# Kernel optimization log

Measured on AMD Instinct MI355X. Metric: run time of the kernel, lower is better.

Reference implementation:

```python
import jax, jax.numpy as jnp
import numpy as np

B, C, H, W = 4, 64, 64, 64
RC, RS = 8, 4  # channel reduction, spatial reduction
CR = C // RC
KS = 2 * RS - 1  # 7


def _conv(x, w, b, stride, pad):
    y = jax.lax.conv_general_dilated(
        x, w, (stride, stride), [(pad, pad), (pad, pad)],
        dimension_numbers=('NCHW', 'OIHW', 'NCHW'))
    return y + b[None, :, None, None]


def setup_inputs() -> dict:
    key = jax.random.key(0)
    ks = jax.random.split(key, 13)

    def w_init(k, shape):
        fan_in = shape[1] * shape[2] * shape[3]
        return jax.random.normal(k, shape, jnp.float32) / jnp.sqrt(fan_in)

    x = jax.random.normal(ks[0], (B, C, H, W), jnp.float32)
    return {
        'x': x,
        'w1': w_init(ks[1], (CR, C, 1, 1)), 'b1': jnp.zeros((CR,), jnp.float32),
        'w2': w_init(ks[2], (CR, C, 1, 1)), 'b2': jnp.zeros((CR,), jnp.float32),
        'w3': w_init(ks[3], (C, C, 1, 1)),  'b3': jnp.zeros((C,), jnp.float32),
        'w4': w_init(ks[4], (C, C, KS, KS)), 'b4': jnp.zeros((C,), jnp.float32),
        'w5': w_init(ks[5], (C, C, KS, KS)), 'b5': jnp.zeros((C,), jnp.float32),
        'w6': w_init(ks[6], (C, C, 1, 1)),  'b6': jnp.zeros((C,), jnp.float32),
    }


def reference(x, w1, b1, w2, b2, w3, b3, w4, b4, w5, b5, w6, b6):
    gamma = 1.0
    x_ori = x
    b, c, h, w = x.shape
    n = h * w

    # ---- Block 1: spatial self-attention (SAGAN-style), N x N scores ----
    f = _conv(x, w1, b1, 1, 0).reshape(b, CR, n)   # [B, C/8, N]
    g = _conv(x, w2, b2, 1, 0).reshape(b, CR, n)   # [B, C/8, N]
    hh = _conv(x, w3, b3, 1, 0).reshape(b, c, n)   # [B, C, N]
    s = jnp.einsum('bci,bcj->bij', f, g)           # [B, N, N] = f^T g
    beta = jax.nn.softmax(s, axis=1)               # softmax over dim 1 (as in torch)
    o = jnp.einsum('bcn,bnm->bcm', hh, beta)       # [B, C, N]
    x2 = o.reshape(b, c, h, w)

    # ---- Block 2: channel attention over strided-conv features, C x C scores ----
    hp, wp = h // RS, w // RS
    npix = hp * wp
    f2 = _conv(x2, w4, b4, RS, RS - 1).reshape(b, c, npix)  # [B, C, N']
    g2 = _conv(x2, w5, b5, RS, RS - 1).reshape(b, c, npix)  # [B, C, N']
    h2 = _conv(x2, w6, b6, 1, 0).reshape(b, c, n)           # [B, C, N]
    s2 = jnp.einsum('bcn,bdn->bcd', f2, g2)                 # [B, C, C] = f g^T
    beta2 = jax.nn.softmax(s2, axis=1)
    # o[b,d,n] = sum_c h2[b,c,n] * beta2[b,c,d]
    o2 = jnp.einsum('bcn,bcd->bdn', h2, beta2).reshape(b, c, h, w)

    return gamma * o2 + x_ori
```

## Files before the change

kernel.cpp:

```cpp
#include <hip/hip_runtime.h>
#include <math.h>

#define BB 4
#define CC 64
#define CRR 8
#define NN 4096

typedef __attribute__((ext_vector_type(8))) short bf16x8;
typedef __attribute__((ext_vector_type(4))) float f32x4;

__device__ inline float bf2f(ushort u) {
    union { uint i; float f; } v; v.i = (uint)u << 16; return v.f;
}
__device__ inline ushort f2bf(float f) {
    uint u = __builtin_bit_cast(uint, f);
    u = (u + 0x7FFFu + ((u >> 16) & 1u)) >> 16;
    return (ushort)u;
}
__device__ inline uint bfpack2(float a, float b) {
    uint ua = __builtin_bit_cast(uint, a);
    uint ub = __builtin_bit_cast(uint, b);
    ua = (ua + 0x7FFFu + ((ua >> 16) & 1u)) >> 16;
    ub = (ub + 0x7FFFu + ((ub >> 16) & 1u)) & 0xFFFF0000u;
    return ua | ub;
}
__device__ inline uint pkrtz(float a, float b) {
    return __builtin_amdgcn_perm(__builtin_bit_cast(uint, b),
                                 __builtin_bit_cast(uint, a), 0x07060302u);
}
__device__ inline float fexp2(float x) { return exp2f(x); }

#define X2P_B 313600

__global__ __launch_bounds__(256) void produce_fgh(
    const float* __restrict__ x,
    const float* __restrict__ w1, const float* __restrict__ b1,
    const float* __restrict__ w2, const float* __restrict__ b2,
    const float* __restrict__ w3, const float* __restrict__ b3,
    ushort* __restrict__ fT, ushort* __restrict__ gT, ushort* __restrict__ hhb)
{
    const float LOG2E = 1.4426950408889634f;
    int t = threadIdx.x;
    int b = blockIdx.x & 3;
    int n = ((blockIdx.x >> 2) << 6) + (t & 63);
    int og = __builtin_amdgcn_readfirstlane(t >> 6);

    const float* xb = x + ((size_t)b << 18) + n;
    float xv[64];
#pragma unroll
    for (int c = 0; c < 64; ++c) xv[c] = xb[(size_t)c << 12];

    if (og == 0) {
        ushort fo[8], go[8];
#pragma unroll
        for (int k = 0; k < 8; ++k) {
            float a1 = b1[k], a2 = b2[k];
#pragma unroll
            for (int c = 0; c < 64; ++c) {
                a1 = fmaf(w1[k * 64 + c], xv[c], a1);
                a2 = fmaf(w2[k * 64 + c], xv[c], a2);
            }
            fo[k] = f2bf(a1 * LOG2E); go[k] = f2bf(a2);
        }
        uint4 fq = make_uint4((uint)fo[0] | ((uint)fo[1] << 16),
                              (uint)fo[2] | ((uint)fo[3] << 16),
                              (uint)fo[4] | ((uint)fo[5] << 16),
                              (uint)fo[6] | ((uint)fo[7] << 16));
        uint4 gq = make_uint4((uint)go[0] | ((uint)go[1] << 16),
                              (uint)go[2] | ((uint)go[3] << 16),
                              (uint)go[4] | ((uint)go[5] << 16),
                              (uint)go[6] | ((uint)go[7] << 16));
        *(uint4*)&fT[((size_t)b << 15) + (size_t)n * 8] = fq;
        *(uint4*)&gT[((size_t)b << 15) + (size_t)n * 8] = gq;
#pragma unroll
        for (int k = 0; k < 4; ++k) {
            float a = b3[k];
#pragma unroll
            for (int c = 0; c < 64; ++c) a = fmaf(w3[k * 64 + c], xv[c], a);
            hhb[((size_t)b << 18) + ((size_t)k << 12) + n] = f2bf(a);
        }
    } else {
        int c0 = og * 20 - 16;
#pragma unroll
        for (int k = 0; k < 20; ++k) {
            float a = b3[c0 + k];
#pragma unroll
            for (int c = 0; c < 64; ++c) a = fmaf(w3[(c0 + k) * 64 + c], xv[c], a);
            hhb[((size_t)b << 18) + ((size_t)(c0 + k) << 12) + n] = f2bf(a);
        }
    }
}

__global__ __launch_bounds__(256) void wtz_kernel(
    const float* __restrict__ w4, const float* __restrict__ w5,
    const float* __restrict__ w6,
    ushort* __restrict__ Wt, ushort* __restrict__ w6b, ushort* __restrict__ x2p)
{
    int bid = blockIdx.x;
    int t = threadIdx.x;
    if (bid < 128) {
        int conv = bid >> 6, co = bid & 63;
        const float* W = conv ? w5 : w4;
        for (int i = t; i < 3136; i += 256) {
            int ci = i / 49, kk = i - ci * 49;
            Wt[(((size_t)(conv * 64 + co)) * 49 + kk) * 64 + ci] = f2bf(W[co * 3136 + i]);
        }
    } else if (bid == 128) {
#pragma unroll
        for (int k = 0; k < 16; ++k) {
            int i = k * 256 + t;
            w6b[i] = f2bf(w6[i]);
        }
    } else {
        int gid = (bid - 129) * 256 + t;
        if (gid >= 4 * 804) return;
        int b = gid / 804;
        int i = gid - b * 804;
        int py, px;
        if (i < 210) { py = i / 70; px = i - py * 70; }
        else if (i < 420) { int j = i - 210; int r = j / 70; py = 67 + r; px = j - r * 70; }
        else { int j = i - 420; int r = j / 6; py = 3 + r; int c = j - r * 6; px = c < 3 ? c : 64 + c; }
        ushort* p = x2p + (size_t)b * X2P_B + (size_t)(py * 70 + px) * 64;
        uint4 z = make_uint4(0, 0, 0, 0);
#pragma unroll
        for (int k = 0; k < 8; ++k) *(uint4*)(p + k * 8) = z;
    }
}

__global__ __launch_bounds__(1024) void attn_kernel(
    const ushort* __restrict__ fT, const ushort* __restrict__ gT,
    const ushort* __restrict__ hhb, const ushort* __restrict__ w6b,
    const float* __restrict__ b6,
    ushort* __restrict__ x2p, ushort* __restrict__ h2b)
{
    __shared__ __align__(16) char smem[98304];
    ushort* hhT = (ushort*)smem;
    ushort* PstB = (ushort*)(smem + 65536);
    float* Acc = (float*)smem;
    float* Lq  = (float*)(smem + 69632);
    ushort* x2s = (ushort*)(smem + 70656);

    int t = threadIdx.x;
    int q = t >> 8, tq = t & 255;
    int l = t & 63;
    int wq = tq >> 6;
    int w16 = t >> 6;
    int ml = l & 15, g = l >> 4;
    int b = blockIdx.x & 3;
    int mt = blockIdx.x >> 2;
    int m0 = mt << 6;
    int col = m0 + wq * 16 + ml;

    const ushort* fTb = fT + ((size_t)b << 15) + (size_t)q * 8192;
    const ushort* gTb = gT + ((size_t)b << 15);
    const ushort* hhB = hhb + ((size_t)b << 18) + (q << 10);

    const bf16x8 z8 = {0, 0, 0, 0, 0, 0, 0, 0};
    const f32x4 z4 = {0.f, 0.f, 0.f, 0.f};

    bf16x8 gfrag = *(const bf16x8*)(gTb + (size_t)col * 8);
    if (g != 0) gfrag = z8;

    int sc = tq >> 2, sp = tq & 3;
    const ushort* hrowBase = hhB + (size_t)sc * 4096 + sp * 16;
    int hdst = q * 8192 + sp * 1024 + sc * 8;

    uint4 h0 = *(const uint4*)(hrowBase);
    uint4 h1 = *(const uint4*)(hrowBase + 8);
    *(uint4*)&hhT[hdst] = h0;
    *(uint4*)&hhT[hdst + 512] = h1;
    bf16x8 afc[4];
#pragma unroll
    for (int s = 0; s < 4; ++s)
        afc[s] = *(const bf16x8*)(fTb + (size_t)(16 * s + ml) * 8);

    f32x4 acc[4] = {z4, z4, z4, z4};
    float rsum = 0.f;
    int swz = (ml & 7) << 4;
    char* pbase = (char*)PstB + w16 * 2048;
    __syncthreads();

    for (int nt = 0; nt < 16; ++nt) {
        int buf = nt & 1;
        bf16x8 afn[4];
        if (nt < 15) {
            int n0 = (nt + 1) << 6;
            h0 = *(const uint4*)(hrowBase + n0);
            h1 = *(const uint4*)(hrowBase + n0 + 8);
#pragma unroll
            for (int s = 0; s < 4; ++s)
                afn[s] = *(const bf16x8*)(fTb + (size_t)(n0 + 16 * s + ml) * 8);
        }

        f32x4 Sv[4];
#pragma unroll
        for (int s = 0; s < 4; ++s)
            Sv[s] = __builtin_amdgcn_mfma_f32_16x16x32_bf16(afc[s], gfrag, z4, 0, 0, 0);

        uint plo[4], phi[4];
#pragma unroll
        for (int s = 0; s < 4; ++s) {
            float p0 = fexp2(Sv[s][0]);
            float p1 = fexp2(Sv[s][1]);
            float p2 = fexp2(Sv[s][2]);
            float p3 = fexp2(Sv[s][3]);
            rsum += (p0 + p1) + (p2 + p3);
            plo[s] = pkrtz(p0, p1);
            phi[s] = pkrtz(p2, p3);
        }

#pragma unroll
        for (int s = 0; s < 4; ++s) {
            uint off = (uint)((ml * 128 + 32 * s + 8 * g) ^ swz);
            *(uint2*)(pbase + off) = make_uint2(plo[s], phi[s]);
        }

#pragma unroll
        for (int kk = 0; kk < 2; ++kk) {
            uint off = (uint)((ml * 128 + 64 * kk + 16 * g) ^ swz);
            bf16x8 pf = *(const bf16x8*)(pbase + off);
#pragma unroll
            for (int ct = 0; ct < 4; ++ct) {
                bf16x8 hf = *(const bf16x8*)&hhT[q * 8192 + buf * 4096 + (kk * 4 + g) * 512 + (16 * ct + ml) * 8];
                acc[ct] = __builtin_amdgcn_mfma_f32_16x16x32_bf16(hf, pf, acc[ct], 0, 0, 0);
            }
        }

        if (nt < 15) {
            int nb = (nt + 1) & 1;
            *(uint4*)&hhT[hdst + nb * 4096] = h0;
            *(uint4*)&hhT[hdst + nb * 4096 + 512] = h1;
#pragma unroll
            for (int s = 0; s < 4; ++s) afc[s] = afn[s];
        }
        __syncthreads();
    }

    rsum += __shfl_xor(rsum, 16);
    rsum += __shfl_xor(rsum, 32);

    {
        float* arow = Acc + q * 4352 + (wq * 16 + ml) * 68;
#pragma unroll
        for (int ct = 0; ct < 4; ++ct)
            *(f32x4*)(arow + 16 * ct + 4 * g) = acc[ct];
        if (g == 0) Lq[q * 64 + wq * 16 + ml] = rsum;
    }
    __syncthreads();

    {
        int m = t >> 4, c0 = (t & 15) << 2;
        float Ltot = Lq[m] + Lq[64 + m] + Lq[128 + m] + Lq[192 + m];
        float rL = 1.f / Ltot;
        f32x4 v0 = *(const f32x4*)(Acc + 0 * 4352 + m * 68 + c0);
        f32x4 v1 = *(const f32x4*)(Acc + 1 * 4352 + m * 68 + c0);
        f32x4 v2 = *(const f32x4*)(Acc + 2 * 4352 + m * 68 + c0);
        f32x4 v3 = *(const f32x4*)(Acc + 3 * 4352 + m * 68 + c0);
        f32x4 v;
#pragma unroll
        for (int r = 0; r < 4; ++r)
            v[r] = ((v0[r] + v1[r]) + (v2[r] + v3[r])) * rL;
        uint2 pk = make_uint2(bfpack2(v[0], v[1]), bfpack2(v[2], v[3]));
        int px = m + 3, py = mt + 3;
        *(uint2*)(x2p + (size_t)b * X2P_B + (size_t)(py * 70 + px) * 64 + c0) = pk;
        *(uint2*)(x2s + m * 72 + c0) = pk;
    }
    __syncthreads();

    {
        int dt = w16 & 3, mq = w16 >> 2;
        f32x4 hacc = z4;
#pragma unroll
        for (int kk = 0; kk < 2; ++kk) {
            bf16x8 xf = *(const bf16x8*)(x2s + (mq * 16 + ml) * 72 + 32 * kk + 8 * g);
            bf16x8 wf = *(const bf16x8*)(w6b + (size_t)(16 * dt + ml) * 64 + 32 * kk + 8 * g);
            hacc = __builtin_amdgcn_mfma_f32_16x16x32_bf16(wf, xf, hacc, 0, 0, 0);
        }
        ushort* h2row = h2b + ((size_t)b << 18) + (m0 + mq * 16 + ml);
#pragma unroll
        for (int r = 0; r < 4; ++r) {
            int d = 16 * dt + 4 * g + r;
            h2row[(size_t)d << 12] = f2bf(hacc[r] + b6[d]);
        }
    }
}

__global__ __launch_bounds__(256) void conv7_split_kernel(
    const ushort* __restrict__ x2p, const ushort* __restrict__ Wt,
    float* __restrict__ part)
{
    int t = threadIdx.x;
    int l = t & 63, w = t >> 6;
    int ml = l & 15, g = l >> 4;
    int lb = (blockIdx.x & 7) * 28 + (blockIdx.x >> 3);
    int bc = lb / 28;
    int idx = (lb % 28) * 4 + w;
    int ky = idx >> 4;
    int ct = (idx >> 2) & 3;
    int og = idx & 3;
    int conv = bc & 1, b = bc >> 1;

    int co0 = ct * 16;
    const ushort* wb = Wt + (size_t)conv * 200704
                     + (size_t)(co0 + ml) * 3136 + (size_t)(ky * 7) * 64 + g * 8;
    const ushort* xbase = x2p + (size_t)b * X2P_B + g * 8;

    int pixoff[4];
#pragma unroll
    for (int s = 0; s < 4; ++s) {
        int opix = og * 64 + s * 16 + ml;
        int oy = opix >> 4, ox = opix & 15;
        pixoff[s] = ((oy * 4 + ky) * 70 + ox * 4) * 64;
    }

    const f32x4 z4 = {0.f, 0.f, 0.f, 0.f};
    f32x4 acc[4] = {z4, z4, z4, z4};

#pragma unroll
    for (int kx = 0; kx < 7; ++kx) {
#pragma unroll
        for (int ci0 = 0; ci0 < 64; ci0 += 32) {
            bf16x8 av = *(const bf16x8*)(wb + kx * 64 + ci0);
#pragma unroll
            for (int s = 0; s < 4; ++s) {
                bf16x8 bv = *(const bf16x8*)(xbase + pixoff[s] + kx * 64 + ci0);
                acc[s] = __builtin_amdgcn_mfma_f32_16x16x32_bf16(av, bv, acc[s], 0, 0, 0);
            }
        }
    }

    float* pb = part + (size_t)(ky * 8 + bc) * 16384;
#pragma unroll
    for (int s = 0; s < 4; ++s) {
        int opix = og * 64 + s * 16 + ml;
#pragma unroll
        for (int r = 0; r < 4; ++r) {
            int co = co0 + 4 * g + r;
            pb[co * 256 + opix] = acc[s][r];
        }
    }
}

__global__ __launch_bounds__(256) void conv7_reduce_kernel(
    const float* __restrict__ part, const float* __restrict__ b4,
    const float* __restrict__ b5, float* __restrict__ f2, float* __restrict__ g2)
{
    int idx = (blockIdx.x * 256 + threadIdx.x) * 4;
    int bc = idx >> 14;
    int co = (idx >> 8) & 63;
    int conv = bc & 1, b = bc >> 1;
    int sub = idx & 16383;
    float4 s = make_float4(0.f, 0.f, 0.f, 0.f);
#pragma unroll
    for (int ky = 0; ky < 7; ++ky) {
        float4 v = *(const float4*)&part[(size_t)(ky * 8 + bc) * 16384 + sub];
        s.x += v.x; s.y += v.y; s.z += v.z; s.w += v.w;
    }
    float bias = (conv ? b5 : b4)[co];
    s.x += bias; s.y += bias; s.z += bias; s.w += bias;
    float* y = conv ? g2 : f2;
    *(float4*)&y[(size_t)b * 16384 + sub] = s;
}

__global__ __launch_bounds__(1024) void s2_softmax_kernel(
    const float* __restrict__ f2, const float* __restrict__ g2,
    float* __restrict__ beta2)
{
    __shared__ __align__(16) float g2t[4][64][68];
    __shared__ __align__(16) float s2f[64][68];
    __shared__ float red[6][64];
    int t = threadIdx.x;
    int b = blockIdx.x;
    int q = t >> 8, tq = t & 255;
    int nb = q * 64;

    {
        int n = tq & 63, c0 = tq >> 6;
#pragma unroll
        for (int k = 0; k < 16; ++k) {
            int cc = c0 * 16 + k;
            g2t[q][n][cc] = g2[((size_t)(b * 64 + cc) << 8) + nb + n];
        }
    }
    __syncthreads();

    int c = tq & 63, dq = tq >> 6, d0 = dq * 16;
    float acc[16];
#pragma unroll
    for (int k = 0; k < 16; ++k) acc[k] = 0.f;
    const float* frow = f2 + ((size_t)(b * 64 + c) << 8) + nb;
#pragma unroll 4
    for (int n = 0; n < 64; ++n) {
        float fv = frow[n];
#pragma unroll
        for (int jj = 0; jj < 4; ++jj) {
            float4 gv = *(const float4*)&g2t[q][n][d0 + jj * 4];
            acc[jj * 4 + 0] = fmaf(fv, gv.x, acc[jj * 4 + 0]);
            acc[jj * 4 + 1] = fmaf(fv, gv.y, acc[jj * 4 + 1]);
            acc[jj * 4 + 2] = fmaf(fv, gv.z, acc[jj * 4 + 2]);
            acc[jj * 4 + 3] = fmaf(fv, gv.w, acc[jj * 4 + 3]);
        }
    }
    __syncthreads();
    float* part = &g2t[0][0][0];
#pragma unroll
    for (int k = 0; k < 16; ++k) part[q * 4096 + c * 64 + d0 + k] = acc[k];
    __syncthreads();
    {
        int idx = t * 4;
        int cc = idx >> 6, dd = idx & 63;
        float4 s0 = *(const float4*)&part[cc * 64 + dd];
        float4 s1 = *(const float4*)&part[4096 + cc * 64 + dd];
        float4 s2v = *(const float4*)&part[8192 + cc * 64 + dd];
        float4 s3 = *(const float4*)&part[12288 + cc * 64 + dd];
        float4 s;
        s.x = (s0.x + s1.x) + (s2v.x + s3.x);
        s.y = (s0.y + s1.y) + (s2v.y + s3.y);
        s.z = (s0.z + s1.z) + (s2v.z + s3.z);
        s.w = (s0.w + s1.w) + (s2v.w + s3.w);
        *(float4*)&s2f[cc][dd] = s;
    }
    __syncthreads();
    if (t < 256) {
        int d = t & 63, cq = t >> 6;
        float mx = -3e38f;
#pragma unroll
        for (int k = 0; k < 16; ++k) mx = fmaxf(mx, s2f[cq * 16 + k][d]);
        red[cq][d] = mx;
    }
    __syncthreads();
    if (t < 64)
        red[4][t] = fmaxf(fmaxf(red[0][t], red[1][t]), fmaxf(red[2][t], red[3][t]));
    __syncthreads();
    if (t < 256) {
        int d = t & 63, cq = t >> 6;
        float mx = red[4][d];
        float s = 0.f;
#pragma unroll
        for (int k = 0; k < 16; ++k) s += __expf(s2f[cq * 16 + k][d] - mx);
        red[cq][d] = s;
    }
    __syncthreads();
    if (t < 64)
        red[5][t] = 1.f / ((red[0][t] + red[1][t]) + (red[2][t] + red[3][t]));
    __syncthreads();
    if (t < 256) {
        int d = t & 63, cq = t >> 6;
        float mx = red[4][d], r = red[5][d];
#pragma unroll
        for (int k = 0; k < 16; ++k) {
            int cc = cq * 16 + k;
            beta2[((size_t)b << 12) + cc * 64 + d] = __expf(s2f[cc][d] - mx) * r;
        }
    }
}

__global__ __launch_bounds__(256) void o2_residual_kernel(
    const ushort* __restrict__ h2b, const float* __restrict__ beta2,
    const float* __restrict__ x, float* __restrict__ out)
{
    __shared__ __align__(16) float b2s[64][64];
    __shared__ float h2s[64][65];
    int t = threadIdx.x;
    int b = blockIdx.x & 3;
    int n0 = (blockIdx.x >> 2) << 6;

    {
#pragma unroll
        for (int k = 0; k < 16; ++k) {
            int idx = k * 256 + t;
            b2s[idx >> 6][idx & 63] = beta2[((size_t)b << 12) + idx];
        }
        int n = t & 63; int c0 = t >> 6;
#pragma unroll
        for (int k = 0; k < 16; ++k) {
            int cc = c0 * 16 + k;
            h2s[cc][n] = bf2f(h2b[((size_t)(b * 64 + cc) << 12) + n0 + n]);
        }
    }
    __syncthreads();

    int n = t & 63, dg = t >> 6, d0 = dg * 16;
    float acc[16];
#pragma unroll
    for (int k = 0; k < 16; ++k) acc[k] = 0.f;

    for (int cc = 0; cc < 64; ++cc) {
        float hv = h2s[cc][n];
#pragma unroll
        for (int jj = 0; jj < 4; ++jj) {
            float4 bv = *reinterpret_cast<const float4*>(&b2s[cc][d0 + jj * 4]);
            acc[jj * 4 + 0] = fmaf(hv, bv.x, acc[jj * 4 + 0]);
            acc[jj * 4 + 1] = fmaf(hv, bv.y, acc[jj * 4 + 1]);
            acc[jj * 4 + 2] = fmaf(hv, bv.z, acc[jj * 4 + 2]);
            acc[jj * 4 + 3] = fmaf(hv, bv.w, acc[jj * 4 + 3]);
        }
    }
#pragma unroll
    for (int k = 0; k < 16; ++k) {
        int d = d0 + k;
        size_t o = ((size_t)(b * 64 + d) << 12) + n0 + n;
        out[o] = acc[k] + x[o];
    }
}

extern "C" void kernel_launch(void* const* d_in, const int* in_sizes, int n_in,
                              void* d_out, int out_size, void* d_ws, size_t ws_size,
                              hipStream_t stream)
{
    const float* x  = (const float*)d_in[0];
    const float* w1 = (const float*)d_in[1];
    const float* b1 = (const float*)d_in[2];
    const float* w2 = (const float*)d_in[3];
    const float* b2 = (const float*)d_in[4];
    const float* w3 = (const float*)d_in[5];
    const float* b3 = (const float*)d_in[6];
    const float* w4 = (const float*)d_in[7];
    const float* b4 = (const float*)d_in[8];
    const float* w5 = (const float*)d_in[9];
    const float* b5 = (const float*)d_in[10];
    const float* w6 = (const float*)d_in[11];
    const float* b6 = (const float*)d_in[12];
    float* out = (float*)d_out;

    ushort* u = (ushort*)d_ws;
    ushort* fT  = u;
    ushort* gT  = fT + 131072;
    ushort* hhb = gT + 131072;
    ushort* x2p = hhb + 1048576;
    ushort* h2b = x2p + 1254400;
    ushort* Wt  = h2b + 1048576;
    ushort* w6b = Wt + 401408;
    float* fr    = (float*)(w6b + 4096);
    float* f2    = fr;
    float* g2    = fr + 65536;
    float* beta2 = fr + 131072;
    float* part  = fr + 147456;

    produce_fgh<<<256, 256, 0, stream>>>(x, w1, b1, w2, b2, w3, b3, fT, gT, hhb);
    wtz_kernel<<<142, 256, 0, stream>>>(w4, w5, w6, Wt, w6b, x2p);
    attn_kernel<<<256, 1024, 0, stream>>>(fT, gT, hhb, w6b, b6, x2p, h2b);
    conv7_split_kernel<<<224, 256, 0, stream>>>(x2p, Wt, part);
    conv7_reduce_kernel<<<128, 256, 0, stream>>>(part, b4, b5, f2, g2);
    s2_softmax_kernel<<<BB, 1024, 0, stream>>>(f2, g2, beta2);
    o2_residual_kernel<<<256, 256, 0, stream>>>(h2b, beta2, x, out);
}
```

Baseline: 86.22 us.

## Split attention into partial-sum and combine kernels; merge weight prep into producer

The 1024-thread attention kernel, which reduced four key-range quarters through shared memory, is replaced by 1024 blocks of 256 threads. Each block writes fp32 partial accumulators and row sums to global memory, and a separate combine kernel sums them, normalizes, writes x2, and runs the w6 1x1 conv. The weight transpose and padding-zero kernel is folded into the producer launch as extra blocks, removing one launch. This trades smaller blocks with more occupancy and less shared memory for about 16MB of extra global partial traffic and one more kernel launch.

```diff
diff --git a/kernel.cpp b/kernel.cpp
--- a/kernel.cpp
+++ b/kernel.cpp
@@ -32,17 +32,53 @@
 
 #define X2P_B 313600
 
-__global__ __launch_bounds__(256) void produce_fgh(
+__global__ __launch_bounds__(256) void produce_wtz_kernel(
     const float* __restrict__ x,
     const float* __restrict__ w1, const float* __restrict__ b1,
     const float* __restrict__ w2, const float* __restrict__ b2,
     const float* __restrict__ w3, const float* __restrict__ b3,
-    ushort* __restrict__ fT, ushort* __restrict__ gT, ushort* __restrict__ hhb)
+    const float* __restrict__ w4, const float* __restrict__ w5,
+    const float* __restrict__ w6,
+    ushort* __restrict__ fT, ushort* __restrict__ gT, ushort* __restrict__ hhb,
+    ushort* __restrict__ Wt, ushort* __restrict__ w6b, ushort* __restrict__ x2p)
 {
     const float LOG2E = 1.4426950408889634f;
     int t = threadIdx.x;
-    int b = blockIdx.x & 3;
-    int n = ((blockIdx.x >> 2) << 6) + (t & 63);
+    int bid0 = blockIdx.x;
+    if (bid0 >= 256) {
+        int bid = bid0 - 256;
+        if (bid < 128) {
+            int conv = bid >> 6, co = bid & 63;
+            const float* W = conv ? w5 : w4;
+            for (int i = t; i < 3136; i += 256) {
+                int ci = i / 49, kk = i - ci * 49;
+                Wt[(((size_t)(conv * 64 + co)) * 49 + kk) * 64 + ci] = f2bf(W[co * 3136 + i]);
+            }
+        } else if (bid == 128) {
+#pragma unroll
+            for (int k = 0; k < 16; ++k) {
+                int i = k * 256 + t;
+                w6b[i] = f2bf(w6[i]);
+            }
+        } else {
+            int gid = (bid - 129) * 256 + t;
+            if (gid >= 4 * 804) return;
+            int b = gid / 804;
+            int i = gid - b * 804;
+            int py, px;
+            if (i < 210) { py = i / 70; px = i - py * 70; }
+            else if (i < 420) { int j = i - 210; int r = j / 70; py = 67 + r; px = j - r * 70; }
+            else { int j = i - 420; int r = j / 6; py = 3 + r; int c = j - r * 6; px = c < 3 ? c : 64 + c; }
+            ushort* p = x2p + (size_t)b * X2P_B + (size_t)(py * 70 + px) * 64;
+            uint4 z = make_uint4(0, 0, 0, 0);
+#pragma unroll
+            for (int k = 0; k < 8; ++k) *(uint4*)(p + k * 8) = z;
+        }
+        return;
+    }
+
+    int b = bid0 & 3;
+    int n = ((bid0 >> 2) << 6) + (t & 63);
     int og = __builtin_amdgcn_readfirstlane(t >> 6);
 
     const float* xb = x + ((size_t)b << 18) + n;
@@ -91,65 +127,23 @@
     }
 }
 
-__global__ __launch_bounds__(256) void wtz_kernel(
-    const float* __restrict__ w4, const float* __restrict__ w5,
-    const float* __restrict__ w6,
-    ushort* __restrict__ Wt, ushort* __restrict__ w6b, ushort* __restrict__ x2p)
-{
+__global__ __launch_bounds__(256) void attn_part_kernel(
+    const ushort* __restrict__ fT, const ushort* __restrict__ gT,
+    const ushort* __restrict__ hhb,
+    float* __restrict__ pacc, float* __restrict__ pL)
+{
+    __shared__ __align__(16) ushort hhT[8192];
+    __shared__ __align__(16) ushort Pst[4096];
+
+    int t = threadIdx.x;
+    int l = t & 63, w = t >> 6;
+    int ml = l & 15, g = l >> 4;
     int bid = blockIdx.x;
-    int t = threadIdx.x;
-    if (bid < 128) {
-        int conv = bid >> 6, co = bid & 63;
-        const float* W = conv ? w5 : w4;
-        for (int i = t; i < 3136; i += 256) {
-            int ci = i / 49, kk = i - ci * 49;
-            Wt[(((size_t)(conv * 64 + co)) * 49 + kk) * 64 + ci] = f2bf(W[co * 3136 + i]);
-        }
-    } else if (bid == 128) {
-#pragma unroll
-        for (int k = 0; k < 16; ++k) {
-            int i = k * 256 + t;
-            w6b[i] = f2bf(w6[i]);
-        }
-    } else {
-        int gid = (bid - 129) * 256 + t;
-        if (gid >= 4 * 804) return;
-        int b = gid / 804;
-        int i = gid - b * 804;
-        int py, px;
-        if (i < 210) { py = i / 70; px = i - py * 70; }
-        else if (i < 420) { int j = i - 210; int r = j / 70; py = 67 + r; px = j - r * 70; }
-        else { int j = i - 420; int r = j / 6; py = 3 + r; int c = j - r * 6; px = c < 3 ? c : 64 + c; }
-        ushort* p = x2p + (size_t)b * X2P_B + (size_t)(py * 70 + px) * 64;
-        uint4 z = make_uint4(0, 0, 0, 0);
-#pragma unroll
-        for (int k = 0; k < 8; ++k) *(uint4*)(p + k * 8) = z;
-    }
-}
-
-__global__ __launch_bounds__(1024) void attn_kernel(
-    const ushort* __restrict__ fT, const ushort* __restrict__ gT,
-    const ushort* __restrict__ hhb, const ushort* __restrict__ w6b,
-    const float* __restrict__ b6,
-    ushort* __restrict__ x2p, ushort* __restrict__ h2b)
-{
-    __shared__ __align__(16) char smem[98304];
-    ushort* hhT = (ushort*)smem;
-    ushort* PstB = (ushort*)(smem + 65536);
-    float* Acc = (float*)smem;
-    float* Lq  = (float*)(smem + 69632);
-    ushort* x2s = (ushort*)(smem + 70656);
-
-    int t = threadIdx.x;
-    int q = t >> 8, tq = t & 255;
-    int l = t & 63;
-    int wq = tq >> 6;
-    int w16 = t >> 6;
-    int ml = l & 15, g = l >> 4;
-    int b = blockIdx.x & 3;
-    int mt = blockIdx.x >> 2;
+    int b = bid & 3;
+    int mt = (bid >> 2) & 63;
+    int q = bid >> 8;
     int m0 = mt << 6;
-    int col = m0 + wq * 16 + ml;
+    int col = m0 + w * 16 + ml;
 
     const ushort* fTb = fT + ((size_t)b << 15) + (size_t)q * 8192;
     const ushort* gTb = gT + ((size_t)b << 15);
@@ -161,9 +155,9 @@
     bf16x8 gfrag = *(const bf16x8*)(gTb + (size_t)col * 8);
     if (g != 0) gfrag = z8;
 
-    int sc = tq >> 2, sp = tq & 3;
+    int sc = t >> 2, sp = t & 3;
     const ushort* hrowBase = hhB + (size_t)sc * 4096 + sp * 16;
-    int hdst = q * 8192 + sp * 1024 + sc * 8;
+    int hdst = sp * 1024 + sc * 8;
 
     uint4 h0 = *(const uint4*)(hrowBase);
     uint4 h1 = *(const uint4*)(hrowBase + 8);
@@ -177,7 +171,7 @@
     f32x4 acc[4] = {z4, z4, z4, z4};
     float rsum = 0.f;
     int swz = (ml & 7) << 4;
-    char* pbase = (char*)PstB + w16 * 2048;
+    char* pbase = (char*)&Pst[0] + w * 2048;
     __syncthreads();
 
     for (int nt = 0; nt < 16; ++nt) {
@@ -221,7 +215,7 @@
             bf16x8 pf = *(const bf16x8*)(pbase + off);
 #pragma unroll
             for (int ct = 0; ct < 4; ++ct) {
-                bf16x8 hf = *(const bf16x8*)&hhT[q * 8192 + buf * 4096 + (kk * 4 + g) * 512 + (16 * ct + ml) * 8];
+                bf16x8 hf = *(const bf16x8*)&hhT[buf * 4096 + (kk * 4 + g) * 512 + (16 * ct + ml) * 8];
                 acc[ct] = __builtin_amdgcn_mfma_f32_16x16x32_bf16(hf, pf, acc[ct], 0, 0, 0);
             }
         }
@@ -240,47 +234,71 @@
     rsum += __shfl_xor(rsum, 32);
 
     {
-        float* arow = Acc + q * 4352 + (wq * 16 + ml) * 68;
+        int m = w * 16 + ml;
+        float* pb = pacc + (size_t)bid * 4096 + m * 64;
 #pragma unroll
         for (int ct = 0; ct < 4; ++ct)
-            *(f32x4*)(arow + 16 * ct + 4 * g) = acc[ct];
-        if (g == 0) Lq[q * 64 + wq * 16 + ml] = rsum;
-    }
-    __syncthreads();
+            *(f32x4*)(pb + 16 * ct + 4 * g) = acc[ct];
+        if (g == 0) pL[(size_t)bid * 64 + m] = rsum;
+    }
+}
+
+__global__ __launch_bounds__(256) void attn_combine_kernel(
+    const float* __restrict__ pacc, const float* __restrict__ pL,
+    const ushort* __restrict__ w6b, const float* __restrict__ b6,
+    ushort* __restrict__ x2p, ushort* __restrict__ h2b)
+{
+    __shared__ __align__(16) ushort x2s[64 * 72];
+    int t = threadIdx.x;
+    int cid = blockIdx.x;
+    int b = cid & 3, mt = cid >> 2;
 
     {
-        int m = t >> 4, c0 = (t & 15) << 2;
-        float Ltot = Lq[m] + Lq[64 + m] + Lq[128 + m] + Lq[192 + m];
-        float rL = 1.f / Ltot;
-        f32x4 v0 = *(const f32x4*)(Acc + 0 * 4352 + m * 68 + c0);
-        f32x4 v1 = *(const f32x4*)(Acc + 1 * 4352 + m * 68 + c0);
-        f32x4 v2 = *(const f32x4*)(Acc + 2 * 4352 + m * 68 + c0);
-        f32x4 v3 = *(const f32x4*)(Acc + 3 * 4352 + m * 68 + c0);
-        f32x4 v;
-#pragma unroll
-        for (int r = 0; r < 4; ++r)
-            v[r] = ((v0[r] + v1[r]) + (v2[r] + v3[r])) * rL;
-        uint2 pk = make_uint2(bfpack2(v[0], v[1]), bfpack2(v[2], v[3]));
+        int m = t >> 2, c0 = (t & 3) << 4;
+        float Lt = 0.f;
+#pragma unroll
+        for (int qq = 0; qq < 4; ++qq) Lt += pL[(size_t)(qq * 256 + cid) * 64 + m];
+        float rL = 1.f / Lt;
+        uint pk[8];
+#pragma unroll
+        for (int k = 0; k < 16; k += 4) {
+            f32x4 s = {0.f, 0.f, 0.f, 0.f};
+#pragma unroll
+            for (int qq = 0; qq < 4; ++qq) {
+                f32x4 p = *(const f32x4*)&pacc[(size_t)(qq * 256 + cid) * 4096 + m * 64 + c0 + k];
+                s += p;
+            }
+            pk[(k >> 1) + 0] = bfpack2(s[0] * rL, s[1] * rL);
+            pk[(k >> 1) + 1] = bfpack2(s[2] * rL, s[3] * rL);
+        }
         int px = m + 3, py = mt + 3;
-        *(uint2*)(x2p + (size_t)b * X2P_B + (size_t)(py * 70 + px) * 64 + c0) = pk;
-        *(uint2*)(x2s + m * 72 + c0) = pk;
+        ushort* xp = x2p + (size_t)b * X2P_B + (size_t)(py * 70 + px) * 64 + c0;
+        *(uint4*)xp = make_uint4(pk[0], pk[1], pk[2], pk[3]);
+        *(uint4*)(xp + 8) = make_uint4(pk[4], pk[5], pk[6], pk[7]);
+        *(uint4*)&x2s[m * 72 + c0] = make_uint4(pk[0], pk[1], pk[2], pk[3]);
+        *(uint4*)&x2s[m * 72 + c0 + 8] = make_uint4(pk[4], pk[5], pk[6], pk[7]);
     }
     __syncthreads();
 
     {
-        int dt = w16 & 3, mq = w16 >> 2;
-        f32x4 hacc = z4;
-#pragma unroll
-        for (int kk = 0; kk < 2; ++kk) {
-            bf16x8 xf = *(const bf16x8*)(x2s + (mq * 16 + ml) * 72 + 32 * kk + 8 * g);
-            bf16x8 wf = *(const bf16x8*)(w6b + (size_t)(16 * dt + ml) * 64 + 32 * kk + 8 * g);
-            hacc = __builtin_amdgcn_mfma_f32_16x16x32_bf16(wf, xf, hacc, 0, 0, 0);
-        }
-        ushort* h2row = h2b + ((size_t)b << 18) + (m0 + mq * 16 + ml);
-#pragma unroll
-        for (int r = 0; r < 4; ++r) {
-            int d = 16 * dt + 4 * g + r;
-            h2row[(size_t)d << 12] = f2bf(hacc[r] + b6[d]);
+        int l = t & 63, w = t >> 6;
+        int ml = l & 15, g = l >> 4;
+        const f32x4 z4 = {0.f, 0.f, 0.f, 0.f};
+#pragma unroll
+        for (int s = 0; s < 4; ++s) {
+            f32x4 hacc = z4;
+#pragma unroll
+            for (int kk = 0; kk < 2; ++kk) {
+                bf16x8 xf = *(const bf16x8*)&x2s[(s * 16 + ml) * 72 + 32 * kk + 8 * g];
+                bf16x8 wf = *(const bf16x8*)(w6b + (size_t)(16 * w + ml) * 64 + 32 * kk + 8 * g);
+                hacc = __builtin_amdgcn_mfma_f32_16x16x32_bf16(wf, xf, hacc, 0, 0, 0);
+            }
+            ushort* h2row = h2b + ((size_t)b << 18) + (mt * 64 + s * 16 + ml);
+#pragma unroll
+            for (int r = 0; r < 4; ++r) {
+                int d = 16 * w + 4 * g + r;
+                h2row[(size_t)d << 12] = f2bf(hacc[r] + b6[d]);
+            }
         }
     }
 }
@@ -536,10 +554,13 @@
     float* g2    = fr + 65536;
     float* beta2 = fr + 131072;
     float* part  = fr + 147456;
-
-    produce_fgh<<<256, 256, 0, stream>>>(x, w1, b1, w2, b2, w3, b3, fT, gT, hhb);
-    wtz_kernel<<<142, 256, 0, stream>>>(w4, w5, w6, Wt, w6b, x2p);
-    attn_kernel<<<256, 1024, 0, stream>>>(fT, gT, hhb, w6b, b6, x2p, h2b);
+    float* pacc  = fr + 1064960;
+    float* pL    = pacc + 4194304;
+
+    produce_wtz_kernel<<<398, 256, 0, stream>>>(x, w1, b1, w2, b2, w3, b3,
+                                                w4, w5, w6, fT, gT, hhb, Wt, w6b, x2p);
+    attn_part_kernel<<<1024, 256, 0, stream>>>(fT, gT, hhb, pacc, pL);
+    attn_combine_kernel<<<256, 256, 0, stream>>>(pacc, pL, w6b, b6, x2p, h2b);
     conv7_split_kernel<<<224, 256, 0, stream>>>(x2p, Wt, part);
     conv7_reduce_kernel<<<128, 256, 0, stream>>>(part, b4, b5, f2, g2);
     s2_softmax_kernel<<<BB, 1024, 0, stream>>>(f2, g2, beta2);
```

Result: slower. 96.73 us (+12.2%).
